# Kernel tuning notes

Measured on AMD Instinct MI355X. Metric: run time of the kernel, lower is better.

The kernel has to match this reference:

```python
import jax, jax.numpy as jnp
import numpy as np

K = 8192      # codebook_dim
D = 256       # embedding_dim
BETA = 0.25
DECAY = 0.99
EPS = 1e-05


def setup_inputs() -> dict:
    key = jax.random.key(0)
    k1, k2, k3, k4 = jax.random.split(key, 4)
    lim = 1.0 / K
    return {
        "z": jax.random.normal(k1, (8, D, 32, 32), dtype=jnp.float32),
        "embedding": jax.random.uniform(k2, (K, D), minval=-lim, maxval=lim, dtype=jnp.float32),
        "cluster_size": jax.random.uniform(k3, (K,), dtype=jnp.float32),
        "ema_w": jax.random.uniform(k4, (K, D), minval=-lim, maxval=lim, dtype=jnp.float32),
    }


def reference(z, embedding, cluster_size, ema_w):
    # z: [B, C, H, W] -> [B, H, W, C]
    zp = jnp.transpose(z, (0, 2, 3, 1))
    zf = zp.reshape(-1, D)                                  # [N, D]
    # squared L2 distance to each code: ||z||^2 + ||e||^2 - 2 z.e
    d = (jnp.sum(zf * zf, axis=1, keepdims=True)
         + jnp.sum(embedding * embedding, axis=1)
         - 2.0 * jnp.einsum("nd,kd->nk", zf, embedding))    # [N, K]
    idx = jnp.argmin(d, axis=1)                             # [N]
    z_q = embedding[idx].reshape(zp.shape)                  # [B, H, W, C]

    # EMA update (training branch), expressed with segment sums instead of
    # materializing the one-hot [N, K] matrix.
    counts = jax.ops.segment_sum(jnp.ones_like(idx, dtype=zf.dtype), idx, num_segments=K)
    new_cs = cluster_size * DECAY + (1.0 - DECAY) * counts
    n = jnp.sum(new_cs)
    new_cs = (new_cs + EPS) / (n + K * EPS) * n
    dw = jax.ops.segment_sum(zf, idx, num_segments=K)       # encodings.T @ zf
    new_ema_w = ema_w * DECAY + (1.0 - DECAY) * dw
    new_embedding = new_ema_w / new_cs[:, None]

    sg = jax.lax.stop_gradient
    loss = jnp.mean((sg(z_q) - zp) ** 2) + BETA * jnp.mean((z_q - sg(zp)) ** 2)
    # straight-through estimator, back to NCHW
    z_q_out = jnp.transpose(zp + sg(z_q - zp), (0, 3, 1, 2))
    return z_q_out, loss, idx, new_cs, new_ema_w, new_embedding
```

## Files before the change

kernel.cpp:

```cpp
#include <hip/hip_runtime.h>

#define CHW 262144
#define HWD 1024

typedef _Float16 v8h __attribute__((ext_vector_type(8)));
typedef _Float16 v4h __attribute__((ext_vector_type(4)));
typedef float    v4f __attribute__((ext_vector_type(4)));

static const unsigned OFF_ASQ  = 0;
static const unsigned OFF_BSQ  = 8192;
static const unsigned OFF_CNT  = 16384;
static const unsigned OFF_HEAD = 24576;
static const unsigned OFF_NXT  = 32768;
static const unsigned OFF_SCAL = 40960;
static const unsigned OFF_AH   = 40968;
static const unsigned OFF_AM   = 1089544;
static const unsigned OFF_BH   = 2138120;
static const unsigned OFF_BM   = 3186696;

#define GLL(g, l) __builtin_amdgcn_global_load_lds( \
    (const __attribute__((address_space(1))) void*)(g), \
    (__attribute__((address_space(3))) void*)(l), 16, 0, 0)

__global__ __launch_bounds__(256) void k_prep(const float* __restrict__ z,
        const float* __restrict__ emb, float* __restrict__ asq, float* __restrict__ bsq,
        _Float16* __restrict__ Bh, _Float16* __restrict__ Bm,
        _Float16* __restrict__ Ah, _Float16* __restrict__ Am,
        float* __restrict__ zerobase) {
    int bx = blockIdx.x;
    int t = threadIdx.x;
    if (bx < 32) {
        int n = bx * 256 + t;
        const float* p = z + (size_t)(n >> 10) * CHW + (n & 1023);
        float s = 0.f;
        #pragma unroll 8
        for (int c = 0; c < 256; ++c) { float v = p[(size_t)c << 10]; s = fmaf(v, v, s); }
        asq[n] = s;
    } else if (bx < 2080) {
        int w = (bx - 32) * 4 + (t >> 6);
        int lane = t & 63;
        float4 v = *(const float4*)(emb + (size_t)w * 256 + lane * 4);
        float s = v.x * v.x;
        s = fmaf(v.y, v.y, s); s = fmaf(v.z, v.z, s); s = fmaf(v.w, v.w, s);
        #pragma unroll
        for (int m = 1; m < 64; m <<= 1) s += __shfl_xor(s, m, 64);
        if (lane == 0) bsq[w] = s;
        float e0 = v.x * 8192.0f, e1 = v.y * 8192.0f, e2 = v.z * 8192.0f, e3 = v.w * 8192.0f;
        _Float16 h0 = (_Float16)e0, h1 = (_Float16)e1, h2 = (_Float16)e2, h3 = (_Float16)e3;
        v4h hv = {h0, h1, h2, h3};
        v4h mv = {(_Float16)((e0 - (float)h0) * 2048.0f),
                  (_Float16)((e1 - (float)h1) * 2048.0f),
                  (_Float16)((e2 - (float)h2) * 2048.0f),
                  (_Float16)((e3 - (float)h3) * 2048.0f)};
        *(v4h*)(Bh + (size_t)w * 256 + lane * 4) = hv;
        *(v4h*)(Bm + (size_t)w * 256 + lane * 4) = mv;
    } else if (bx < 2592) {
        __shared__ float s[64][65];
        int blk = bx - 2080;
        int hw0 = (blk & 15) * 64;
        int c0  = ((blk >> 4) & 3) * 64;
        int b   = blk >> 6;
        #pragma unroll
        for (int ii = 0; ii < 16; ++ii) {
            int e = t + ii * 256;
            int c = e >> 6, x = e & 63;
            s[c][x] = z[(size_t)b * CHW + (size_t)(c0 + c) * HWD + hw0 + x];
        }
        __syncthreads();
        int n = t & 63, cseg = (t >> 6) * 16;
        _Float16 hbuf[16], mbuf[16];
        #pragma unroll
        for (int j = 0; j < 16; ++j) {
            float v = s[cseg + j][n];
            _Float16 h = (_Float16)v;
            float r = v - (float)h;
            hbuf[j] = h;
            mbuf[j] = (_Float16)(r * 2048.0f);
        }
        size_t off = ((size_t)b * 1024 + hw0 + n) * 256 + c0 + cseg;
        *(v8h*)(Ah + off)     = *(v8h*)(hbuf);
        *(v8h*)(Ah + off + 8) = *(v8h*)(hbuf + 8);
        *(v8h*)(Am + off)     = *(v8h*)(mbuf);
        *(v8h*)(Am + off + 8) = *(v8h*)(mbuf + 8);
    } else {
        int idx = (bx - 2592) * 1024 + t * 4;
        *(float4*)(zerobase + idx) = (float4){0.f, 0.f, 0.f, 0.f};
        if (bx == 2592 && t == 0)
            *(float4*)(zerobase + 24576) = (float4){0.f, 0.f, 0.f, 0.f};
    }
}

__global__ __launch_bounds__(512, 2) void k_main(
        const _Float16* __restrict__ Ah, const _Float16* __restrict__ Am,
        const _Float16* __restrict__ Bh, const _Float16* __restrict__ Bm,
        const float* __restrict__ asq, const float* __restrict__ bsq,
        unsigned* __restrict__ pdk) {
    __shared__ _Float16 lds[32768];
    const int bid = blockIdx.x;
    const int xcd = bid & 7, s = bid >> 3;
    const int rect = s >> 5, rr = s & 31;
    const int rg = xcd * 8 + rect;
    const int nt = (rg & 7) * 4 + (rr >> 3);
    const int kt = (rg >> 3) * 8 + (rr & 7);
    const int n0 = nt * 256, k0 = kt * 128;
    const int t = threadIdx.x;
    const int lane = t & 63, w = t >> 6;
    const int wrow = w >> 1, wcol = w & 1;
    const int lm = lane & 15, quad = lane >> 4;

    v4f acc1[4][4], acc2[4][4];
    #pragma unroll
    for (int i = 0; i < 4; ++i)
        #pragma unroll
        for (int j = 0; j < 4; ++j) { acc1[i][j] = (v4f){0.f,0.f,0.f,0.f}; acc2[i][j] = (v4f){0.f,0.f,0.f,0.f}; }

    const int row0 = t >> 2;
    const int c40 = (t & 3) ^ ((row0 >> 1) & 3);
    const char* gA  = (const char*)Ah + (size_t)(n0 + row0) * 512 + c40 * 16;
    const char* gAm = (const char*)Am + (size_t)(n0 + row0) * 512 + c40 * 16;
    const char* gB  = (const char*)Bh + (size_t)(k0 + row0) * 512 + c40 * 16;
    const char* gBm = (const char*)Bm + (size_t)(k0 + row0) * 512 + c40 * 16;

    int sa[4], sb[4];
    #pragma unroll
    for (int i = 0; i < 4; ++i) {
        int mr = wrow * 64 + i * 16 + lm;
        sa[i] = mr * 32 + ((quad ^ ((mr >> 1) & 3)) * 8);
    }
    #pragma unroll
    for (int j = 0; j < 4; ++j) {
        int nr = wcol * 64 + j * 16 + lm;
        sb[j] = nr * 32 + ((quad ^ ((nr >> 1) & 3)) * 8);
    }

    auto stageA = [&](int cb) {
        const size_t co = (size_t)cb * 64;
        _Float16* l = lds + t * 8;
        GLL(gA + co,           l);
        GLL(gA + co + 65536,   l + 4096);
        GLL(gAm + co,          l + 8192);
        GLL(gAm + co + 65536,  l + 12288);
    };
    auto stageB = [&](int cb, int buf) {
        const size_t co = (size_t)cb * 64;
        _Float16* l = lds + 16384 + buf * 8192 + t * 8;
        GLL(gB + co,  l);
        GLL(gBm + co, l + 4096);
    };

#define MFMA16(A, B, C) __builtin_amdgcn_mfma_f32_16x16x32_f16(A, B, C, 0, 0, 0)
#define PROD(I, J, FA, FAM, FB, FBM) do { \
        acc1[I][J] = MFMA16(FA,  FB,  acc1[I][J]); \
        acc2[I][J] = MFMA16(FA,  FBM, acc2[I][J]); \
        acc2[I][J] = MFMA16(FAM, FB,  acc2[I][J]); \
    } while (0)

    stageA(0);
    stageB(0, 0);
    for (int cb = 0; cb < 8; ++cb) {
        asm volatile("s_waitcnt vmcnt(0)" ::: "memory");
        __builtin_amdgcn_s_barrier();
        __builtin_amdgcn_sched_barrier(0);
        if (cb < 7) stageB(cb + 1, (cb + 1) & 1);
        const _Float16* LB = lds + 16384 + (cb & 1) * 8192;

        v8h fa0  = *(const v8h*)(lds + sa[0]);
        v8h fa1  = *(const v8h*)(lds + sa[1]);
        v8h fa2  = *(const v8h*)(lds + sa[2]);
        v8h fa3  = *(const v8h*)(lds + sa[3]);
        v8h fam0 = *(const v8h*)(lds + 8192 + sa[0]);
        v8h fam1 = *(const v8h*)(lds + 8192 + sa[1]);
        v8h fam2 = *(const v8h*)(lds + 8192 + sa[2]);
        v8h fam3 = *(const v8h*)(lds + 8192 + sa[3]);
        v8h fb0  = *(const v8h*)(LB + sb[0]);
        v8h fb1  = *(const v8h*)(LB + sb[1]);
        v8h fbm0 = *(const v8h*)(LB + 4096 + sb[0]);
        v8h fbm1 = *(const v8h*)(LB + 4096 + sb[1]);

        __builtin_amdgcn_s_setprio(1);
        PROD(0, 0, fa0, fam0, fb0, fbm0);
        PROD(0, 1, fa0, fam0, fb1, fbm1);
        PROD(1, 0, fa1, fam1, fb0, fbm0);
        PROD(1, 1, fa1, fam1, fb1, fbm1);
        PROD(2, 0, fa2, fam2, fb0, fbm0);
        PROD(2, 1, fa2, fam2, fb1, fbm1);
        PROD(3, 0, fa3, fam3, fb0, fbm0);
        PROD(3, 1, fa3, fam3, fb1, fbm1);
        __builtin_amdgcn_s_setprio(0);
        __builtin_amdgcn_sched_barrier(0);

        asm volatile("s_waitcnt lgkmcnt(0)" ::: "memory");
        __builtin_amdgcn_s_barrier();
        __builtin_amdgcn_sched_barrier(0);
        if (cb < 7) stageA(cb + 1);

        v8h fb2  = *(const v8h*)(LB + sb[2]);
        v8h fb3  = *(const v8h*)(LB + sb[3]);
        v8h fbm2 = *(const v8h*)(LB + 4096 + sb[2]);
        v8h fbm3 = *(const v8h*)(LB + 4096 + sb[3]);

        __builtin_amdgcn_s_setprio(1);
        PROD(0, 2, fa0, fam0, fb2, fbm2);
        PROD(0, 3, fa0, fam0, fb3, fbm3);
        PROD(1, 2, fa1, fam1, fb2, fbm2);
        PROD(1, 3, fa1, fam1, fb3, fbm3);
        PROD(2, 2, fa2, fam2, fb2, fbm2);
        PROD(2, 3, fa2, fam2, fb3, fbm3);
        PROD(3, 2, fa3, fam3, fb2, fbm2);
        PROD(3, 3, fa3, fam3, fb3, fbm3);
        __builtin_amdgcn_s_setprio(0);
        __builtin_amdgcn_sched_barrier(0);
    }
#undef PROD
#undef MFMA16

    float bvv[4];
    #pragma unroll
    for (int j = 0; j < 4; ++j) bvv[j] = bsq[k0 + wcol * 64 + j * 16 + lm];
    __syncthreads();
    unsigned* lrow = (unsigned*)lds;
    #pragma unroll
    for (int i = 0; i < 4; ++i) {
        #pragma unroll
        for (int r = 0; r < 4; ++r) {
            int mm = wrow * 64 + i * 16 + quad * 4 + r;
            float av_ = asq[n0 + mm];
            unsigned best = 0xFFFFFFFFu;
            #pragma unroll
            for (int j = 0; j < 4; ++j) {
                float S = fmaf(acc2[i][j][r], 4.8828125e-4f, acc1[i][j][r]) * 1.220703125e-4f;
                float dd = (av_ + bvv[j]) - 2.0f * S;
                float gv = dd - av_;
                int mi = (int)(gv * 65536.0f) + 32768;
                int col = k0 + wcol * 64 + j * 16 + lm;
                unsigned key = ((unsigned)mi << 13) | (unsigned)col;
                best = key < best ? key : best;
            }
            #pragma unroll
            for (int xm = 1; xm < 16; xm <<= 1) {
                unsigned o = __shfl_xor(best, xm, 64);
                best = o < best ? o : best;
            }
            if (lm == 0) lrow[wcol * 256 + mm] = best;
        }
    }
    __syncthreads();
    {
        int mm2 = t & 255, half = t >> 8;
        pdk[((size_t)(nt * 2 + (mm2 >> 7)) * 128 + kt * 2 + half) * 128 + (mm2 & 127)]
            = lrow[half * 256 + mm2];
    }
}

__global__ __launch_bounds__(256) void k_zqr(const unsigned* __restrict__ pdk,
        const float* __restrict__ z, const float* __restrict__ emb, const float* __restrict__ cs,
        float* __restrict__ out_idx, int* __restrict__ cnt,
        int* __restrict__ head, int* __restrict__ nxt,
        float* __restrict__ out_zq, float* __restrict__ scal) {
    const int bx = blockIdx.x, by = blockIdx.y;
    const int n0 = bx * 64, c00 = by * 64;
    const int lane = threadIdx.x & 63, g = threadIdx.x >> 6;
    const int nt = bx >> 1, mb = (bx & 1) * 64;

    unsigned mn = 0xFFFFFFFFu;
    const unsigned* base = pdk + (((size_t)nt * 128 + g * 32) << 7) + mb + lane;
    #pragma unroll 8
    for (int jj = 0; jj < 32; ++jj) {
        unsigned key = base[jj << 7];
        mn = key < mn ? key : mn;
    }
    __shared__ unsigned part[4][64];
    part[g][lane] = mn;
    __syncthreads();
    unsigned k0v = part[0][lane], k1v = part[1][lane];
    unsigned k2v = part[2][lane], k3v = part[3][lane];
    unsigned f01 = k0v < k1v ? k0v : k1v;
    unsigned f23 = k2v < k3v ? k2v : k3v;
    unsigned fkey = f01 < f23 ? f01 : f23;
    int idxn = (int)(fkey & 8191u);
    int n = n0 + lane;

    if (by == 0) {
        if (g == 0) {
            out_idx[n] = (float)idxn;
            atomicAdd(cnt + idxn, 1);
            int old = atomicExch(head + idxn, n + 1);
            nxt[n] = old;
        } else if (g == 1) {
            float cv = cs[n];
            #pragma unroll
            for (int m = 1; m < 64; m <<= 1) cv += __shfl_xor(cv, m, 64);
            if (lane == 0) atomicAdd(scal + 1, cv);
        }
    }

    int b = n >> 10, hw = n & 1023;
    const float* zr = z + (size_t)b * CHW + hw;
    const float* er = emb + (size_t)idxn * 256;
    float* oz = out_zq + (size_t)b * CHW + hw;
    float ls = 0.f;
    #pragma unroll
    for (int q = 0; q < 4; ++q) {
        int c = c00 + g * 16 + q * 4;
        float4 e4 = *(const float4*)(er + c);
        float ev[4] = {e4.x, e4.y, e4.z, e4.w};
        #pragma unroll
        for (int r = 0; r < 4; ++r) {
            float zp = zr[(size_t)(c + r) << 10];
            float dif = ev[r] - zp;
            oz[(size_t)(c + r) << 10] = zp + dif;
            ls = fmaf(dif, dif, ls);
        }
    }
    #pragma unroll
    for (int m = 1; m < 64; m <<= 1) ls += __shfl_xor(ls, m, 64);
    __shared__ float red[4];
    if (lane == 0) red[g] = ls;
    __syncthreads();
    if (threadIdx.x == 0) atomicAdd(scal, red[0] + red[1] + red[2] + red[3]);
}

__global__ __launch_bounds__(256) void k_fin(const float* __restrict__ cs, const float* __restrict__ ema,
        const int* __restrict__ head, const int* __restrict__ nxt,
        const _Float16* __restrict__ Ah, const _Float16* __restrict__ Am,
        const float* __restrict__ scal, const int* __restrict__ cnt,
        float* __restrict__ out_ncs, float* __restrict__ out_ema,
        float* __restrict__ out_emb, float* __restrict__ out_loss) {
    int k = blockIdx.x * 4 + (threadIdx.x >> 6);
    int lane = threadIdx.x & 63;
    float4 dwv = {0.f, 0.f, 0.f, 0.f};
    int cur = head[k];
    while (cur) {
        int n = cur - 1;
        v4h hh = *(const v4h*)(Ah + (size_t)n * 256 + lane * 4);
        v4h mm = *(const v4h*)(Am + (size_t)n * 256 + lane * 4);
        dwv.x += fmaf((float)mm[0], 4.8828125e-4f, (float)hh[0]);
        dwv.y += fmaf((float)mm[1], 4.8828125e-4f, (float)hh[1]);
        dwv.z += fmaf((float)mm[2], 4.8828125e-4f, (float)hh[2]);
        dwv.w += fmaf((float)mm[3], 4.8828125e-4f, (float)hh[3]);
        cur = nxt[n];
    }
    const float C1 = (float)(1.0 - 0.99);
    const float KEPS = (float)(8192 * 1e-5);
    float ncs0v = cs[k] * 0.99f + C1 * (float)cnt[k];
    float nsum = 0.99f * scal[1] + C1 * 8192.0f;
    float ncs = (ncs0v + 1e-5f) / (nsum + KEPS) * nsum;
    if (lane == 0) out_ncs[k] = ncs;
    size_t base = (size_t)k * 256 + lane * 4;
    float4 e4 = *(const float4*)(ema + base);
    float r0 = e4.x * 0.99f + C1 * dwv.x;
    float r1 = e4.y * 0.99f + C1 * dwv.y;
    float r2 = e4.z * 0.99f + C1 * dwv.z;
    float r3 = e4.w * 0.99f + C1 * dwv.w;
    out_ema[base + 0] = r0; out_ema[base + 1] = r1; out_ema[base + 2] = r2; out_ema[base + 3] = r3;
    out_emb[base + 0] = r0 / ncs; out_emb[base + 1] = r1 / ncs;
    out_emb[base + 2] = r2 / ncs; out_emb[base + 3] = r3 / ncs;
    if (blockIdx.x == 0 && threadIdx.x == 0) {
        float m = scal[0] * (1.0f / 2097152.0f);
        out_loss[0] = m + 0.25f * m;
    }
}

extern "C" void kernel_launch(void* const* d_in, const int* in_sizes, int n_in,
                              void* d_out, int out_size, void* d_ws, size_t ws_size,
                              hipStream_t stream) {
    const float* z   = (const float*)d_in[0];
    const float* emb = (const float*)d_in[1];
    const float* cs  = (const float*)d_in[2];
    const float* ema = (const float*)d_in[3];
    float* out = (float*)d_out;
    float* wsf = (float*)d_ws;

    float* asq  = wsf + OFF_ASQ;
    float* bsq  = wsf + OFF_BSQ;
    int*   cnt  = (int*)(wsf + OFF_CNT);
    int*   head = (int*)(wsf + OFF_HEAD);
    int*   nxt  = (int*)(wsf + OFF_NXT);
    float* scal = wsf + OFF_SCAL;
    _Float16* Ah = (_Float16*)(wsf + OFF_AH);
    _Float16* Am = (_Float16*)(wsf + OFF_AM);
    _Float16* Bh = (_Float16*)(wsf + OFF_BH);
    _Float16* Bm = (_Float16*)(wsf + OFF_BM);

    float* out_zq   = out;
    float* out_loss = out + 2097152;
    float* out_idx  = out + 2097153;
    float* out_ncs  = out + 2105345;
    float* out_ema  = out + 2113537;
    float* out_emb  = out + 4210689;

    unsigned* pdk = (unsigned*)(out + 2113540);

    k_prep<<<2608, 256, 0, stream>>>(z, emb, asq, bsq, Bh, Bm, Ah, Am, wsf + OFF_CNT);
    k_main<<<2048, 512, 0, stream>>>(Ah, Am, Bh, Bm, asq, bsq, pdk);
    k_zqr<<<dim3(128, 4), 256, 0, stream>>>(pdk, z, emb, cs, out_idx, cnt, head, nxt, out_zq, scal);
    k_fin<<<2048, 256, 0, stream>>>(cs, ema, head, nxt, Ah, Am, scal, cnt, out_ncs, out_ema, out_emb, out_loss);
}
```

Before: 245.4 us.

## Triple-buffer A and B tiles in LDS with prefetch two stages ahead

Replaces the single A buffer plus double-buffered B scheme with a three-stage ring in which A and B are loaded together two k-steps ahead. Each iteration now needs one barrier instead of two, and it waits with a partial vmcnt so one stage's loads stay in flight. LDS use grows from 64 KB to 144 KB per block, which with launch_bounds(512,2) may reduce the number of resident blocks per CU.

New measurement: 241.9 us. Within noise of the previous version (-1.4%).

```diff
diff --git a/kernel.cpp b/kernel.cpp
--- a/kernel.cpp
+++ b/kernel.cpp
@@ -95,7 +95,7 @@
         const _Float16* __restrict__ Bh, const _Float16* __restrict__ Bm,
         const float* __restrict__ asq, const float* __restrict__ bsq,
         unsigned* __restrict__ pdk) {
-    __shared__ _Float16 lds[32768];
+    __shared__ _Float16 lds[73728];
     const int bid = blockIdx.x;
     const int xcd = bid & 7, s = bid >> 3;
     const int rect = s >> 5, rr = s & 31;
@@ -133,19 +133,15 @@
         sb[j] = nr * 32 + ((quad ^ ((nr >> 1) & 3)) * 8);
     }
 
-    auto stageA = [&](int cb) {
+    auto stage = [&](int cb, int buf) {
         const size_t co = (size_t)cb * 64;
-        _Float16* l = lds + t * 8;
+        _Float16* l = lds + buf * 24576 + t * 8;
         GLL(gA + co,           l);
         GLL(gA + co + 65536,   l + 4096);
         GLL(gAm + co,          l + 8192);
         GLL(gAm + co + 65536,  l + 12288);
-    };
-    auto stageB = [&](int cb, int buf) {
-        const size_t co = (size_t)cb * 64;
-        _Float16* l = lds + 16384 + buf * 8192 + t * 8;
-        GLL(gB + co,  l);
-        GLL(gBm + co, l + 4096);
+        GLL(gB + co,           l + 16384);
+        GLL(gBm + co,          l + 20480);
     };
 
 #define MFMA16(A, B, C) __builtin_amdgcn_mfma_f32_16x16x32_f16(A, B, C, 0, 0, 0)
@@ -155,27 +151,29 @@
         acc2[I][J] = MFMA16(FAM, FB,  acc2[I][J]); \
     } while (0)
 
-    stageA(0);
-    stageB(0, 0);
+    stage(0, 0);
+    stage(1, 1);
+    #pragma unroll
     for (int cb = 0; cb < 8; ++cb) {
-        asm volatile("s_waitcnt vmcnt(0)" ::: "memory");
+        if (cb < 7) { asm volatile("s_waitcnt vmcnt(6)" ::: "memory"); }
+        else        { asm volatile("s_waitcnt vmcnt(0)" ::: "memory"); }
         __builtin_amdgcn_s_barrier();
         __builtin_amdgcn_sched_barrier(0);
-        if (cb < 7) stageB(cb + 1, (cb + 1) & 1);
-        const _Float16* LB = lds + 16384 + (cb & 1) * 8192;
-
-        v8h fa0  = *(const v8h*)(lds + sa[0]);
-        v8h fa1  = *(const v8h*)(lds + sa[1]);
-        v8h fa2  = *(const v8h*)(lds + sa[2]);
-        v8h fa3  = *(const v8h*)(lds + sa[3]);
-        v8h fam0 = *(const v8h*)(lds + 8192 + sa[0]);
-        v8h fam1 = *(const v8h*)(lds + 8192 + sa[1]);
-        v8h fam2 = *(const v8h*)(lds + 8192 + sa[2]);
-        v8h fam3 = *(const v8h*)(lds + 8192 + sa[3]);
-        v8h fb0  = *(const v8h*)(LB + sb[0]);
-        v8h fb1  = *(const v8h*)(LB + sb[1]);
-        v8h fbm0 = *(const v8h*)(LB + 4096 + sb[0]);
-        v8h fbm1 = *(const v8h*)(LB + 4096 + sb[1]);
+        if (cb < 6) stage(cb + 2, (cb + 2) % 3);
+        const _Float16* L = lds + (cb % 3) * 24576;
+
+        v8h fa0  = *(const v8h*)(L + sa[0]);
+        v8h fa1  = *(const v8h*)(L + sa[1]);
+        v8h fa2  = *(const v8h*)(L + sa[2]);
+        v8h fa3  = *(const v8h*)(L + sa[3]);
+        v8h fam0 = *(const v8h*)(L + 8192 + sa[0]);
+        v8h fam1 = *(const v8h*)(L + 8192 + sa[1]);
+        v8h fam2 = *(const v8h*)(L + 8192 + sa[2]);
+        v8h fam3 = *(const v8h*)(L + 8192 + sa[3]);
+        v8h fb0  = *(const v8h*)(L + 16384 + sb[0]);
+        v8h fb1  = *(const v8h*)(L + 16384 + sb[1]);
+        v8h fbm0 = *(const v8h*)(L + 20480 + sb[0]);
+        v8h fbm1 = *(const v8h*)(L + 20480 + sb[1]);
 
         __builtin_amdgcn_s_setprio(1);
         PROD(0, 0, fa0, fam0, fb0, fbm0);
@@ -187,17 +185,11 @@
         PROD(3, 0, fa3, fam3, fb0, fbm0);
         PROD(3, 1, fa3, fam3, fb1, fbm1);
         __builtin_amdgcn_s_setprio(0);
-        __builtin_amdgcn_sched_barrier(0);
-
-        asm volatile("s_waitcnt lgkmcnt(0)" ::: "memory");
-        __builtin_amdgcn_s_barrier();
-        __builtin_amdgcn_sched_barrier(0);
-        if (cb < 7) stageA(cb + 1);
-
-        v8h fb2  = *(const v8h*)(LB + sb[2]);
-        v8h fb3  = *(const v8h*)(LB + sb[3]);
-        v8h fbm2 = *(const v8h*)(LB + 4096 + sb[2]);
-        v8h fbm3 = *(const v8h*)(LB + 4096 + sb[3]);
+
+        v8h fb2  = *(const v8h*)(L + 16384 + sb[2]);
+        v8h fb3  = *(const v8h*)(L + 16384 + sb[3]);
+        v8h fbm2 = *(const v8h*)(L + 20480 + sb[2]);
+        v8h fbm3 = *(const v8h*)(L + 20480 + sb[3]);
 
         __builtin_amdgcn_s_setprio(1);
         PROD(0, 2, fa0, fam0, fb2, fbm2);
@@ -209,7 +201,6 @@
         PROD(3, 2, fa3, fam3, fb2, fbm2);
         PROD(3, 3, fa3, fam3, fb3, fbm3);
         __builtin_amdgcn_s_setprio(0);
-        __builtin_amdgcn_sched_barrier(0);
     }
 #undef PROD
 #undef MFMA16
```
